# Performance work log

Measured on AMD Instinct MI355X. Metric: run time of the kernel, lower is better.

## Reference

```python
import jax, jax.numpy as jnp
import numpy as np

B, S1, S2, D1, D2 = 4, 2048, 2048, 512, 512
H, DK, DV = 8, 64, 64


def setup_inputs() -> dict:
    key = jax.random.key(0)
    ks = jax.random.split(key, 8)
    x1 = jax.random.normal(ks[0], (B, S1, D1), dtype=jnp.float32)
    x2 = jax.random.normal(ks[1], (B, S2, D2), dtype=jnp.float32)
    x3 = jax.random.normal(ks[2], (B, S2, D2), dtype=jnp.float32)
    s = 0.02
    Wq = jax.random.normal(ks[3], (D1, H * DK), dtype=jnp.float32) * s
    Wk = jax.random.normal(ks[4], (D2, H * DK), dtype=jnp.float32) * s
    Wv = jax.random.normal(ks[5], (D2, H * DV), dtype=jnp.float32) * s
    Wo = jax.random.normal(ks[6], (H * DV, D1), dtype=jnp.float32) * s
    bo = jnp.zeros((D1,), dtype=jnp.float32)
    return {"x1": x1, "x2": x2, "x3": x3, "Wq": Wq, "Wk": Wk, "Wv": Wv, "Wo": Wo, "bo": bo}


def reference(x1, x2, x3, Wq, Wk, Wv, Wo, bo):
    b, s1, _ = x1.shape
    # project to per-head q, k, v: [B, H, S, Dh]
    q = (x1 @ Wq).reshape(b, s1, H, DK).transpose(0, 2, 1, 3)
    k = (x2 @ Wk).reshape(b, x2.shape[1], H, DK).transpose(0, 2, 1, 3)
    v = (x3 @ Wv).reshape(b, x3.shape[1], H, DV).transpose(0, 2, 1, 3)
    scores = jnp.einsum('bhqd,bhkd->bhqk', q, k) / jnp.sqrt(jnp.float32(DK))
    attn = jax.nn.softmax(scores, axis=-1)
    out = jnp.einsum('bhqk,bhkd->bhqd', attn, v)  # [B, H, S1, DV]
    out = out.transpose(0, 2, 1, 3).reshape(b, s1, H * DV)
    return out @ Wo + bo
```

## Files before the change

### kernel.cpp

```cpp
#include <hip/hip_runtime.h>

typedef __attribute__((ext_vector_type(4))) float f32x4;
typedef __attribute__((ext_vector_type(8))) __bf16 bf16x8;
typedef __attribute__((ext_vector_type(4))) __bf16 bf16x4;

#define DEVINL __device__ __forceinline__

DEVINL void gld16(const void* g, void* l) {
  __builtin_amdgcn_global_load_lds((__attribute__((address_space(1))) void*)(void*)g,
                                   (__attribute__((address_space(3))) void*)l, 16, 0, 0);
}


__global__ __launch_bounds__(256) void cvt_all(const float* x1, const float* x2, const float* x3,
                                               const float* Wq, const float* Wk, const float* Wv,
                                               const float* Wo, __bf16* o0, __bf16* o1, __bf16* o2,
                                               __bf16* WT) {
  __shared__ float t[64][65];
  const int bx = blockIdx.x;
  if (bx < 12288) {
    const int z = bx >> 12;
    const float* s = z == 0 ? x1 : z == 1 ? x2 : x3;
    __bf16* d = z == 0 ? o0 : z == 1 ? o1 : o2;
    size_t i = (size_t)(bx & 4095) * 256 + threadIdx.x;
    f32x4 v = ((const f32x4*)s)[i];
    bf16x4 o;
#pragma unroll
    for (int j = 0; j < 4; ++j) o[j] = (__bf16)v[j];
    ((bf16x4*)d)[i] = o;
  } else {
    const int l = bx - 12288;
    const int z = l >> 6;
    const float* W = z == 0 ? Wq : z == 1 ? Wk : z == 2 ? Wv : Wo;
    __bf16* D = WT + (size_t)z * 512 * 512;
    const int r0 = ((l >> 3) & 7) * 64, c0 = (l & 7) * 64;
    const int tx = threadIdx.x & 63, ty = threadIdx.x >> 6;
#pragma unroll
    for (int j = 0; j < 16; ++j)
      t[ty + j * 4][tx] = W[(size_t)(r0 + ty + j * 4) * 512 + c0 + tx];
    __syncthreads();
#pragma unroll
    for (int j = 0; j < 16; ++j)
      D[(size_t)(c0 + ty + j * 4) * 512 + r0 + tx] = (__bf16)t[tx][ty + j * 4];
  }
}


DEVINL void gemm_tile(const __bf16* A, const __bf16* Bt, int m0, int n0,
                      __bf16* As, __bf16* Bs, f32x4 acc[4][4]) {
  const int tid = threadIdx.x, lane = tid & 63, w = tid >> 6;
  const int qd = lane >> 4, r = lane & 15;
  const int wm = w & 1, wn = w >> 1;
  const char* ap[4];
  const char* bp[4];
#pragma unroll
  for (int j = 0; j < 4; ++j) {
    int c = (w * 4 + j) * 64 + lane;
    int row = c >> 3, cs = c & 7;
    int gc = cs ^ (row & 7);
    ap[j] = (const char*)A + (size_t)(m0 + row) * 1024 + gc * 16;
    bp[j] = (const char*)Bt + (size_t)(n0 + row) * 1024 + gc * 16;
  }
  int offA[4][2], offB[4][2];
#pragma unroll
  for (int t = 0; t < 4; ++t)
#pragma unroll
    for (int ks = 0; ks < 2; ++ks) {
      int m = wm * 64 + t * 16 + r;
      offA[t][ks] = m * 128 + (((ks * 4 + qd) ^ (m & 7)) * 16);
      int n = wn * 64 + t * 16 + r;
      offB[t][ks] = n * 128 + (((ks * 4 + qd) ^ (n & 7)) * 16);
    }
  char* AsC = (char*)As;
  char* BsC = (char*)Bs;
  for (int kt = 0; kt < 8; ++kt) {
    __syncthreads();
#pragma unroll
    for (int j = 0; j < 4; ++j) {
      gld16(ap[j] + kt * 128, AsC + (w * 4 + j) * 1024);
      gld16(bp[j] + kt * 128, BsC + (w * 4 + j) * 1024);
    }
    __syncthreads();
#pragma unroll
    for (int ks = 0; ks < 2; ++ks) {
      bf16x8 a[4], b[4];
#pragma unroll
      for (int t = 0; t < 4; ++t) {
        a[t] = *(const bf16x8*)(AsC + offA[t][ks]);
        b[t] = *(const bf16x8*)(BsC + offB[t][ks]);
      }
#pragma unroll
      for (int i = 0; i < 4; ++i)
#pragma unroll
        for (int j2 = 0; j2 < 4; ++j2)
          acc[i][j2] = __builtin_amdgcn_mfma_f32_16x16x32_bf16(a[i], b[j2], acc[i][j2], 0, 0, 0);
    }
  }
}

__global__ __launch_bounds__(256, 3) void gemm_proj(const __bf16* x1b, const __bf16* x2b,
                                                    const __bf16* x3b, const __bf16* WT,
                                                    __bf16* Qo, __bf16* Ko, __bf16* Vto) {
  __shared__ __align__(16) char smem[34816];
  __bf16* As = (__bf16*)smem;
  __bf16* Bs = (__bf16*)(smem + 16384);
  const int z = blockIdx.z;
  const __bf16* A = z == 0 ? x1b : z == 1 ? x2b : x3b;
  const __bf16* Bt = WT + (size_t)z * 512 * 512;
  const int l = blockIdx.x;
  const int sidx = l >> 3;
  const int m0 = ((l & 7) * 8 + (sidx >> 2)) * 128;
  const int n0 = (sidx & 3) * 128;
  f32x4 acc[4][4] = {};
  gemm_tile(A, Bt, m0, n0, As, Bs, acc);
  const int tid = threadIdx.x, lane = tid & 63, w = tid >> 6;
  const int qd = lane >> 4, r = lane & 15, wm = w & 1, wn = w >> 1;
  const int b = m0 >> 11, sbase = m0 & 2047;
  if (z == 2) {
    __syncthreads();
    char* T = smem;
#pragma unroll
    for (int mt = 0; mt < 4; ++mt)
#pragma unroll
      for (int nt = 0; nt < 4; ++nt) {
        int dv = wn * 64 + nt * 16 + r;
        int sl = wm * 64 + mt * 16 + qd * 4;
        bf16x4 p4;
#pragma unroll
        for (int g = 0; g < 4; ++g) p4[g] = (__bf16)acc[mt][nt][g];
        *(bf16x4*)(T + (size_t)dv * 272 + sl * 2) = p4;
      }
    __syncthreads();
#pragma unroll
    for (int p2 = 0; p2 < 2; ++p2) {
      int dvrow = p2 * 64 + (tid >> 2);
      int col = n0 + dvrow, h = col >> 6, d = col & 63;
      __bf16* dst = Vto + ((size_t)(b * 8 + h) * 64 + d) * 2048 + sbase + (tid & 3) * 8;
#pragma unroll
      for (int j = 0; j < 4; ++j) {
        bf16x8 vv = *(const bf16x8*)(T + (size_t)dvrow * 272 + (tid & 3) * 16 + j * 64);
        *(bf16x8*)(dst + j * 32) = vv;
      }
    }
  } else {
    const float qscale = 0.18033688f;
#pragma unroll
    for (int mt = 0; mt < 4; ++mt) {
#pragma unroll
      for (int nt = 0; nt < 4; ++nt) {
        f32x4 v = acc[mt][nt];
        if (z == 0) {
#pragma unroll
          for (int g = 0; g < 4; ++g) v[g] *= qscale;
        }
        int col = n0 + wn * 64 + nt * 16 + r;
        int h = col >> 6, d = col & 63;
        int s = sbase + wm * 64 + mt * 16 + qd * 4;
        __bf16* O = (z == 0 ? Qo : Ko) + ((size_t)(b * 8 + h) * 2048 + s) * 64 + d;
#pragma unroll
        for (int g = 0; g < 4; ++g) O[(size_t)g * 64] = (__bf16)v[g];
      }
    }
  }
}

__global__ __launch_bounds__(256, 2) void gemm_out(const __bf16* Ob, const __bf16* WoT,
                                                   const float* bo, float* out) {
  __shared__ __align__(16) __bf16 As[64 * 64];
  __shared__ __align__(16) __bf16 Bs[128 * 64];
  const int tid = threadIdx.x, lane = tid & 63, w = tid >> 6;
  const int qd = lane >> 4, r = lane & 15, wm = w & 1, wn = w >> 1;
  const int id = blockIdx.x;
  const int rest = id >> 3;
  const int m0 = ((id & 7) * 16 + (rest & 15)) * 64;
  const int n0 = (rest >> 4) * 128;
  const char* ap[2];
  const char* bp[4];
#pragma unroll
  for (int j = 0; j < 2; ++j) {
    int c = (w * 2 + j) * 64 + lane;
    int row = c >> 3, gc = (c & 7) ^ (row & 7);
    ap[j] = (const char*)Ob + (size_t)(m0 + row) * 1024 + gc * 16;
  }
#pragma unroll
  for (int j = 0; j < 4; ++j) {
    int c = (w * 4 + j) * 64 + lane;
    int row = c >> 3, gc = (c & 7) ^ (row & 7);
    bp[j] = (const char*)WoT + (size_t)(n0 + row) * 1024 + gc * 16;
  }
  int offA[2][2], offB[4][2];
#pragma unroll
  for (int ks = 0; ks < 2; ++ks) {
#pragma unroll
    for (int t = 0; t < 2; ++t) {
      int m = wm * 32 + t * 16 + r;
      offA[t][ks] = m * 128 + (((ks * 4 + qd) ^ (m & 7)) * 16);
    }
#pragma unroll
    for (int t = 0; t < 4; ++t) {
      int n = wn * 64 + t * 16 + r;
      offB[t][ks] = n * 128 + (((ks * 4 + qd) ^ (n & 7)) * 16);
    }
  }
  char* AsC = (char*)As;
  char* BsC = (char*)Bs;
  f32x4 acc[2][4] = {};
  for (int kt = 0; kt < 8; ++kt) {
    __syncthreads();
#pragma unroll
    for (int j = 0; j < 2; ++j) gld16(ap[j] + kt * 128, AsC + (w * 2 + j) * 1024);
#pragma unroll
    for (int j = 0; j < 4; ++j) gld16(bp[j] + kt * 128, BsC + (w * 4 + j) * 1024);
    __syncthreads();
#pragma unroll
    for (int ks = 0; ks < 2; ++ks) {
      bf16x8 a[2], b[4];
#pragma unroll
      for (int t = 0; t < 2; ++t) a[t] = *(const bf16x8*)(AsC + offA[t][ks]);
#pragma unroll
      for (int t = 0; t < 4; ++t) b[t] = *(const bf16x8*)(BsC + offB[t][ks]);
#pragma unroll
      for (int i = 0; i < 2; ++i)
#pragma unroll
        for (int j2 = 0; j2 < 4; ++j2)
          acc[i][j2] = __builtin_amdgcn_mfma_f32_16x16x32_bf16(a[i], b[j2], acc[i][j2], 0, 0, 0);
    }
  }
#pragma unroll
  for (int nt = 0; nt < 4; ++nt) {
    int col = n0 + wn * 64 + nt * 16 + r;
    float bv = bo[col];
#pragma unroll
    for (int mt = 0; mt < 2; ++mt) {
      int mg = m0 + wm * 32 + mt * 16 + qd * 4;
#pragma unroll
      for (int g = 0; g < 4; ++g) out[(size_t)(mg + g) * 512 + col] = acc[mt][nt][g] + bv;
    }
  }
}

__global__ __launch_bounds__(256, 4) void attn(const __bf16* Q, const __bf16* K,
                                               const __bf16* Vt, __bf16* Opart, float* Lp) {
  __shared__ __align__(16) __bf16 QPs[128 * 64];
  __shared__ __align__(16) __bf16 Ks[64 * 64];
  __shared__ __align__(16) __bf16 Vs[64 * 64];
  const int tid = threadIdx.x, lane = tid & 63, w = tid >> 6;
  const int qd = lane >> 4, r = lane & 15;
  const int id = blockIdx.x;
  const int rest = id >> 3;
  const int bh = (id & 7) * 4 + (rest >> 5);
  const int kvh = (rest >> 4) & 1;
  const int q0 = (rest & 15) * 128;
  const __bf16* Qg = Q + ((size_t)bh * 2048 + q0) * 64;
  const __bf16* Kg = K + (size_t)bh * 2048 * 64;
  const __bf16* Vg = Vt + (size_t)bh * 64 * 2048;
  char* PsC = (char*)QPs;
  char* KsC = (char*)Ks;
  char* VsC = (char*)Vs;

#pragma unroll
  for (int j = 0; j < 4; ++j) {
    int c = (w * 4 + j) * 64 + lane;
    int m = c >> 3, gc = (c & 7) ^ (m & 7);
    gld16((const char*)Qg + m * 128 + gc * 16, PsC + (w * 4 + j) * 1024);
  }
  __syncthreads();

  bf16x8 qf[2][2];
#pragma unroll
  for (int mt = 0; mt < 2; ++mt)
#pragma unroll
    for (int ks = 0; ks < 2; ++ks) {
      int m = w * 32 + mt * 16 + r;
      qf[mt][ks] = *(const bf16x8*)(PsC + m * 128 + ((ks * 4 + qd) ^ (m & 7)) * 16);
    }

  int offKV[4][2];
#pragma unroll
  for (int t = 0; t < 4; ++t)
#pragma unroll
    for (int ks = 0; ks < 2; ++ks) {
      int n = t * 16 + r;
      offKV[t][ks] = n * 128 + ((ks * 4 + qd) ^ (n & 7)) * 16;
    }

  bf16x8 ones;
#pragma unroll
  for (int j = 0; j < 8; ++j) ones[j] = (__bf16)1.0f;

  f32x4 oacc[2][4] = {};
  f32x4 lacc[2] = {};

  const int kt0 = kvh * 16;
  for (int kt = kt0; kt < kt0 + 16; ++kt) {
    __syncthreads();
#pragma unroll
    for (int j = 0; j < 2; ++j) {
      int c = (w * 2 + j) * 64 + lane;
      int m = c >> 3, gc = (c & 7) ^ (m & 7);
      gld16((const char*)Kg + (size_t)(kt * 64 + m) * 128 + gc * 16, KsC + (w * 2 + j) * 1024);
      gld16((const char*)Vg + (size_t)m * 4096 + kt * 128 + gc * 16, VsC + (w * 2 + j) * 1024);
    }
    __syncthreads();

    f32x4 sf[2][4] = {};
#pragma unroll
    for (int nt = 0; nt < 4; ++nt) {
      bf16x8 kf0 = *(const bf16x8*)(KsC + offKV[nt][0]);
      bf16x8 kf1 = *(const bf16x8*)(KsC + offKV[nt][1]);
#pragma unroll
      for (int mt = 0; mt < 2; ++mt) {
        sf[mt][nt] = __builtin_amdgcn_mfma_f32_16x16x32_bf16(kf0, qf[mt][0], sf[mt][nt], 0, 0, 0);
        sf[mt][nt] = __builtin_amdgcn_mfma_f32_16x16x32_bf16(kf1, qf[mt][1], sf[mt][nt], 0, 0, 0);
      }
    }
#pragma unroll
    for (int mt = 0; mt < 2; ++mt) {
      int q = w * 32 + mt * 16 + r;
#pragma unroll
      for (int nt = 0; nt < 4; ++nt) {
        bf16x4 p4;
#pragma unroll
        for (int g = 0; g < 4; ++g) p4[g] = (__bf16)__builtin_exp2f(sf[mt][nt][g]);
        *(bf16x4*)(PsC + q * 128 + (((2 * nt + (qd >> 1)) ^ (q & 7)) * 16) + (qd & 1) * 8) = p4;
      }
    }
#pragma unroll
    for (int mt = 0; mt < 2; ++mt) {
      int q = w * 32 + mt * 16 + r;
      bf16x8 pf0 = *(const bf16x8*)(PsC + q * 128 + ((qd ^ (q & 7)) * 16));
      bf16x8 pf1 = *(const bf16x8*)(PsC + q * 128 + (((4 + qd) ^ (q & 7)) * 16));
      lacc[mt] = __builtin_amdgcn_mfma_f32_16x16x32_bf16(pf0, ones, lacc[mt], 0, 0, 0);
      lacc[mt] = __builtin_amdgcn_mfma_f32_16x16x32_bf16(pf1, ones, lacc[mt], 0, 0, 0);
#pragma unroll
      for (int dvt = 0; dvt < 4; ++dvt) {
        bf16x8 vf0 = *(const bf16x8*)(VsC + offKV[dvt][0]);
        bf16x8 vf1 = *(const bf16x8*)(VsC + offKV[dvt][1]);
        oacc[mt][dvt] = __builtin_amdgcn_mfma_f32_16x16x32_bf16(pf0, vf0, oacc[mt][dvt], 0, 0, 0);
        oacc[mt][dvt] = __builtin_amdgcn_mfma_f32_16x16x32_bf16(pf1, vf1, oacc[mt][dvt], 0, 0, 0);
      }
    }
  }

  const size_t pbase = (size_t)(kvh * 32 + bh) * 2048;
#pragma unroll
  for (int mt = 0; mt < 2; ++mt) {
    if (r == 0) {
#pragma unroll
      for (int g = 0; g < 4; ++g)
        Lp[pbase + q0 + w * 32 + mt * 16 + qd * 4 + g] = lacc[mt][g];
    }
  }
  __bf16* Ob0 = Opart + pbase * 64;
#pragma unroll
  for (int mt = 0; mt < 2; ++mt) {
#pragma unroll
    for (int g = 0; g < 4; ++g) {
      int s = q0 + w * 32 + mt * 16 + qd * 4 + g;
#pragma unroll
      for (int dvt = 0; dvt < 4; ++dvt)
        Ob0[(size_t)s * 64 + dvt * 16 + r] = (__bf16)oacc[mt][dvt][g];
    }
  }
}

__global__ __launch_bounds__(256) void combine(const __bf16* Op, const float* Lp, __bf16* Ob) {
  int c = blockIdx.x * 256 + threadIdx.x;
  int bhs = c >> 3;
  int dv0 = (c & 7) * 8;
  size_t e = (size_t)bhs * 64 + dv0;
  bf16x8 a = *(const bf16x8*)(Op + e);
  bf16x8 b2 = *(const bf16x8*)(Op + ((size_t)32 * 2048 * 64) + e);
  float inv = 1.0f / (Lp[bhs] + Lp[bhs + 65536]);
  int bh = bhs >> 11, s = bhs & 2047, b = bh >> 3, h = bh & 7;
  bf16x8 o;
#pragma unroll
  for (int j = 0; j < 8; ++j) o[j] = (__bf16)(((float)a[j] + (float)b2[j]) * inv);
  *(bf16x8*)(Ob + ((size_t)(b * 2048 + s)) * 512 + h * 64 + dv0) = o;
}


extern "C" void kernel_launch(void* const* d_in, const int* in_sizes, int n_in,
                              void* d_out, int out_size, void* d_ws, size_t ws_size,
                              hipStream_t stream) {
  const float* x1 = (const float*)d_in[0];
  const float* x2 = (const float*)d_in[1];
  const float* x3 = (const float*)d_in[2];
  const float* Wq = (const float*)d_in[3];
  const float* Wk = (const float*)d_in[4];
  const float* Wv = (const float*)d_in[5];
  const float* Wo = (const float*)d_in[6];
  const float* bo = (const float*)d_in[7];
  float* out = (float*)d_out;
  char* ws = (char*)d_ws;
  const size_t MB = 1ull << 20;
  __bf16* x1b = (__bf16*)(ws);
  __bf16* x2b = (__bf16*)(ws + 8 * MB);
  __bf16* x3b = (__bf16*)(ws + 16 * MB);
  __bf16* WT = (__bf16*)(ws + 24 * MB);
  __bf16* Qb = (__bf16*)(ws + 26 * MB);
  __bf16* Kb = (__bf16*)(ws + 34 * MB);
  __bf16* Vtb = (__bf16*)(ws + 42 * MB);
  __bf16* Ob = (__bf16*)(ws + 50 * MB);
  __bf16* Opart = (__bf16*)(ws + 58 * MB);
  float* Lp = (float*)(ws + 74 * MB);

  cvt_all<<<dim3(12544), 256, 0, stream>>>(x1, x2, x3, Wq, Wk, Wv, Wo, x1b, x2b, x3b, WT);
  gemm_proj<<<dim3(256, 1, 3), 256, 0, stream>>>(x1b, x2b, x3b, WT, Qb, Kb, Vtb);
  attn<<<dim3(1024), 256, 0, stream>>>(Qb, Kb, Vtb, Opart, Lp);
  combine<<<dim3(2048), 256, 0, stream>>>(Opart, Lp, Ob);
  gemm_out<<<dim3(512), 256, 0, stream>>>(Ob, WT + 3ull * 512 * 512, bo, out);
}
```

Measured before the change: 193.4 us.

## Double-buffer K tiles and prefetch next tile during attention compute

The K tile in shared memory is double-buffered. The next K tile is prefetched while the current one is consumed, and the V load is issued at loop start so it overlaps with the QK^T and exp work. One of the two barriers per iteration moves to sit between the P write and the PV stage, and the loop is manually unrolled by two to alternate buffers. This costs 8KB more LDS per block, which may reduce occupancy, and the synchronisation correctness depends on the load ordering of global_load_lds.

```diff
diff --git a/kernel.cpp b/kernel.cpp
--- a/kernel.cpp
+++ b/kernel.cpp
@@ -242,7 +242,7 @@
 __global__ __launch_bounds__(256, 4) void attn(const __bf16* Q, const __bf16* K,
                                                const __bf16* Vt, __bf16* Opart, float* Lp) {
   __shared__ __align__(16) __bf16 QPs[128 * 64];
-  __shared__ __align__(16) __bf16 Ks[64 * 64];
+  __shared__ __align__(16) __bf16 Ksd[2][64 * 64];
   __shared__ __align__(16) __bf16 Vs[64 * 64];
   const int tid = threadIdx.x, lane = tid & 63, w = tid >> 6;
   const int qd = lane >> 4, r = lane & 15;
@@ -255,8 +255,23 @@
   const __bf16* Kg = K + (size_t)bh * 2048 * 64;
   const __bf16* Vg = Vt + (size_t)bh * 64 * 2048;
   char* PsC = (char*)QPs;
-  char* KsC = (char*)Ks;
+  char* Ks0 = (char*)Ksd;
+  char* Ks1 = (char*)Ksd + 8192;
   char* VsC = (char*)Vs;
+
+  const char* Kst[2];
+  const char* Vst[2];
+  int ldso[2];
+#pragma unroll
+  for (int j = 0; j < 2; ++j) {
+    int c = (w * 2 + j) * 64 + lane;
+    int m = c >> 3, gc = (c & 7) ^ (m & 7);
+    Kst[j] = (const char*)Kg + (size_t)m * 128 + gc * 16;
+    Vst[j] = (const char*)Vg + (size_t)m * 4096 + gc * 16;
+    ldso[j] = (w * 2 + j) * 1024;
+  }
+
+  const int kt0 = kvh * 16;
 
 #pragma unroll
   for (int j = 0; j < 4; ++j) {
@@ -264,6 +279,8 @@
     int m = c >> 3, gc = (c & 7) ^ (m & 7);
     gld16((const char*)Qg + m * 128 + gc * 16, PsC + (w * 4 + j) * 1024);
   }
+#pragma unroll
+  for (int j = 0; j < 2; ++j) gld16(Kst[j] + (size_t)kt0 * 8192, Ks0 + ldso[j]);
   __syncthreads();
 
   bf16x8 qf[2][2];
@@ -287,31 +304,28 @@
   bf16x8 ones;
 #pragma unroll
   for (int j = 0; j < 8; ++j) ones[j] = (__bf16)1.0f;
+  const f32x4 z4 = {};
 
   f32x4 oacc[2][4] = {};
   f32x4 lacc[2] = {};
 
-  const int kt0 = kvh * 16;
-  for (int kt = kt0; kt < kt0 + 16; ++kt) {
+  auto iter = [&](int kt, int ktn, char* Kc, char* Kn) {
     __syncthreads();
 #pragma unroll
     for (int j = 0; j < 2; ++j) {
-      int c = (w * 2 + j) * 64 + lane;
-      int m = c >> 3, gc = (c & 7) ^ (m & 7);
-      gld16((const char*)Kg + (size_t)(kt * 64 + m) * 128 + gc * 16, KsC + (w * 2 + j) * 1024);
-      gld16((const char*)Vg + (size_t)m * 4096 + kt * 128 + gc * 16, VsC + (w * 2 + j) * 1024);
-    }
-    __syncthreads();
-
-    f32x4 sf[2][4] = {};
+      gld16(Vst[j] + (size_t)kt * 128, VsC + ldso[j]);
+      gld16(Kst[j] + (size_t)ktn * 8192, Kn + ldso[j]);
+    }
+
+    f32x4 sf[2][4];
 #pragma unroll
     for (int nt = 0; nt < 4; ++nt) {
-      bf16x8 kf0 = *(const bf16x8*)(KsC + offKV[nt][0]);
-      bf16x8 kf1 = *(const bf16x8*)(KsC + offKV[nt][1]);
+      bf16x8 kf0 = *(const bf16x8*)(Kc + offKV[nt][0]);
+      bf16x8 kf1 = *(const bf16x8*)(Kc + offKV[nt][1]);
 #pragma unroll
       for (int mt = 0; mt < 2; ++mt) {
-        sf[mt][nt] = __builtin_amdgcn_mfma_f32_16x16x32_bf16(kf0, qf[mt][0], sf[mt][nt], 0, 0, 0);
-        sf[mt][nt] = __builtin_amdgcn_mfma_f32_16x16x32_bf16(kf1, qf[mt][1], sf[mt][nt], 0, 0, 0);
+        f32x4 t0 = __builtin_amdgcn_mfma_f32_16x16x32_bf16(kf0, qf[mt][0], z4, 0, 0, 0);
+        sf[mt][nt] = __builtin_amdgcn_mfma_f32_16x16x32_bf16(kf1, qf[mt][1], t0, 0, 0, 0);
       }
     }
 #pragma unroll
@@ -325,6 +339,9 @@
         *(bf16x4*)(PsC + q * 128 + (((2 * nt + (qd >> 1)) ^ (q & 7)) * 16) + (qd & 1) * 8) = p4;
       }
     }
+
+    __syncthreads();
+
 #pragma unroll
     for (int mt = 0; mt < 2; ++mt) {
       int q = w * 32 + mt * 16 + r;
@@ -340,6 +357,13 @@
         oacc[mt][dvt] = __builtin_amdgcn_mfma_f32_16x16x32_bf16(pf1, vf1, oacc[mt][dvt], 0, 0, 0);
       }
     }
+  };
+
+#pragma unroll 1
+  for (int kt = kt0; kt < kt0 + 16; kt += 2) {
+    iter(kt, kt + 1, Ks0, Ks1);
+    int kt2 = (kt + 2 < kt0 + 16) ? kt + 2 : kt + 1;
+    iter(kt + 1, kt2, Ks1, Ks0);
   }
 
   const size_t pbase = (size_t)(kvh * 32 + bh) * 2048;
```

New measurement: 189.9 us. About the same (-1.8%).
